# Kernel optimization log

Measured on AMD Instinct MI355X. Metric: run time of the kernel, lower is better.

The kernel has to match this reference:

```python
import jax, jax.numpy as jnp
import numpy as np

B, L, S, D, H = 2, 2048, 2048, 1024, 16
DK = D // H  # d_keys = d_values = 64


def setup_inputs() -> dict:
    key = jax.random.key(0)
    ks = jax.random.split(key, 12)
    sc = 0.02
    return {
        "queries": jax.random.normal(ks[0], (B, L, D), jnp.float32),
        "keys": jax.random.normal(ks[1], (B, S, D), jnp.float32),
        "values": jax.random.normal(ks[2], (B, S, D), jnp.float32),
        "attn_mask": jnp.ones((L, S), dtype=bool),
        "Wq": jax.random.normal(ks[3], (D, H * DK), jnp.float32) * sc,
        "bq": jnp.zeros((H * DK,), jnp.float32),
        "Wk": jax.random.normal(ks[4], (D, H * DK), jnp.float32) * sc,
        "bk": jnp.zeros((H * DK,), jnp.float32),
        "Wv": jax.random.normal(ks[5], (D, H * DK), jnp.float32) * sc,
        "bv": jnp.zeros((H * DK,), jnp.float32),
        "Wo": jax.random.normal(ks[6], (H * DK, D), jnp.float32) * sc,
        "bo": jnp.zeros((D,), jnp.float32),
    }


def reference(queries, keys, values, attn_mask, Wq, bq, Wk, bk, Wv, bv, Wo, bo):
    b, l, _ = queries.shape
    s = keys.shape[1]
    # QKV projections -> [B, T, H, DK]
    q = (queries @ Wq + bq).reshape(b, l, H, DK)
    k = (keys @ Wk + bk).reshape(b, s, H, DK)
    v = (values @ Wv + bv).reshape(b, s, H, DK)
    scale = 1.0 / jnp.sqrt(jnp.asarray(DK, q.dtype))
    # attention scores [B, H, L, S]
    scores = jnp.einsum("blhd,bshd->bhls", q, k) * scale
    scores = jnp.where(attn_mask[None, None, :, :], scores, jnp.finfo(scores.dtype).min)
    attn = jax.nn.softmax(scores, axis=-1)
    out = jnp.einsum("bhls,bshd->blhd", attn, v).reshape(b, l, H * DK)
    out = out @ Wo + bo
    return (out, attn)
```

## Files before the change

### kernel.cpp

```cpp
#include <hip/hip_runtime.h>
#include <hip/hip_bf16.h>


#define BB 2
#define LL 2048
#define SS 2048
#define DD 1024
#define HH 16
#define DKK 64

typedef __bf16 bf16_t;
typedef bf16_t bf16x8 __attribute__((ext_vector_type(8)));
typedef bf16_t bf16x4 __attribute__((ext_vector_type(4)));
typedef float f32x4 __attribute__((ext_vector_type(4)));

static __device__ __forceinline__ f32x4 mfma16(bf16x8 a, bf16x8 b, f32x4 c) {
  return __builtin_amdgcn_mfma_f32_16x16x32_bf16(a, b, c, 0, 0, 0);
}

__global__ void wconv_kernel(const float* __restrict__ Wq, const float* __restrict__ Wk,
                             const float* __restrict__ Wv, const float* __restrict__ Wo,
                             bf16_t* __restrict__ wT) {
  const int which = blockIdx.z;
  const float* W = (which == 0) ? Wq : (which == 1) ? Wk : (which == 2) ? Wv : Wo;
  bf16_t* dst = wT + (size_t)which * 1024 * 1024;
  __shared__ float tile[32][33];
  const int n0 = blockIdx.x * 32, k0 = blockIdx.y * 32;
  const int tx = threadIdx.x, ty = threadIdx.y;
#pragma unroll
  for (int i = 0; i < 4; i++) {
    int k = ty * 4 + i;
    tile[k][tx] = W[(size_t)(k0 + k) * 1024 + n0 + tx];
  }
  __syncthreads();
#pragma unroll
  for (int i = 0; i < 4; i++) {
    int n = ty * 4 + i;
    dst[(size_t)(n0 + n) * 1024 + k0 + tx] = (bf16_t)tile[tx][n];
  }
}

__global__ void aconv_kernel(const float* __restrict__ q, const float* __restrict__ k,
                             const float* __restrict__ v, bf16_t* __restrict__ out) {
  const int which = blockIdx.y;
  const float* src = (which == 0) ? q : (which == 1) ? k : v;
  bf16_t* dst = out + (size_t)which * 4 * 1024 * 1024;
  const size_t i = ((size_t)blockIdx.x * 256 + threadIdx.x) * 4;
  float4 f = *(const float4*)(src + i);
  bf16x4 t;
  t[0] = (bf16_t)f.x; t[1] = (bf16_t)f.y; t[2] = (bf16_t)f.z; t[3] = (bf16_t)f.w;
  *(bf16x4*)(dst + i) = t;
}

__launch_bounds__(256)
__global__ void qkv_gemm_kernel(const bf16_t* __restrict__ abf, const bf16_t* __restrict__ wT,
                                const float* __restrict__ bq, const float* __restrict__ bk,
                                const float* __restrict__ bv, bf16_t* __restrict__ q_ws,
                                bf16_t* __restrict__ k_ws, bf16_t* __restrict__ v_ws) {
  const int which = blockIdx.z;
  const bf16_t* A = abf + (size_t)which * 4 * 1024 * 1024;
  const bf16_t* BT = wT + (size_t)which * 1024 * 1024;
  const float* bias = (which == 0) ? bq : (which == 1) ? bk : bv;
  bf16_t* out = (which == 0) ? q_ws : (which == 1) ? k_ws : v_ws;

  const int n_blk = blockIdx.x * 128, m_blk = blockIdx.y * 128;
  const int lane = threadIdx.x & 63, w = threadIdx.x >> 6;
  const int wm = m_blk + (w >> 1) * 64, wn = n_blk + (w & 1) * 64;
  const int r = lane & 15, quad = lane >> 4;

  f32x4 acc[4][4] = {};
  for (int k0 = 0; k0 < 1024; k0 += 32) {
    const int kq = k0 + quad * 8;
    bf16x8 af[4], bfv[4];
#pragma unroll
    for (int mi = 0; mi < 4; mi++)
      af[mi] = *(const bf16x8*)(A + (size_t)(wm + mi * 16 + r) * 1024 + kq);
#pragma unroll
    for (int ni = 0; ni < 4; ni++)
      bfv[ni] = *(const bf16x8*)(BT + (size_t)(wn + ni * 16 + r) * 1024 + kq);
#pragma unroll
    for (int mi = 0; mi < 4; mi++)
#pragma unroll
      for (int ni = 0; ni < 4; ni++) acc[mi][ni] = mfma16(af[mi], bfv[ni], acc[mi][ni]);
  }
#pragma unroll
  for (int ni = 0; ni < 4; ni++) {
    const int n = wn + ni * 16 + r;
    const float bs = bias[n];
    const int h = n >> 6, d = n & 63;
#pragma unroll
    for (int mi = 0; mi < 4; mi++) {
#pragma unroll
      for (int reg = 0; reg < 4; reg++) {
        const int m = wm + mi * 16 + quad * 4 + reg;
        const int b = m >> 11, t = m & 2047;
        out[((size_t)(b * HH + h) * SS + t) * DKK + d] = (bf16_t)(acc[mi][ni][reg] + bs);
      }
    }
  }
}

__global__ void vtrans_kernel(const bf16_t* __restrict__ v, bf16_t* __restrict__ vT) {
  const int bh = blockIdx.y, s0 = blockIdx.x * 64;
  __shared__ bf16_t tile[64][68];
  const int t = threadIdx.x;
  {
    const int row = t >> 2, cb = (t & 3) * 16;
    const bf16_t* src = v + ((size_t)bh * SS + s0 + row) * DKK + cb;
#pragma unroll
    for (int i = 0; i < 16; i++) tile[row][cb + i] = src[i];
  }
  __syncthreads();
  {
    const int d = t >> 2, sb = (t & 3) * 16;
    bf16_t* dst = vT + ((size_t)bh * DKK + d) * SS + s0 + sb;
#pragma unroll
    for (int i = 0; i < 16; i++) dst[i] = tile[sb + i][d];
  }
}

__launch_bounds__(256, 4)
__global__ void attn_kernel(const bf16_t* __restrict__ q_ws, const bf16_t* __restrict__ k_ws,
                            const bf16_t* __restrict__ vT_ws, float* __restrict__ attn_out,
                            bf16_t* __restrict__ ao_ws) {
  const int lin = blockIdx.x;
  const int xcd = lin & 7;
  const int idx = lin >> 3;
  const int bh = (xcd << 2) | (idx >> 5);
  const int xblk = idx & 31;
  const int b = bh >> 4, h = bh & 15;
  const int tid = threadIdx.x, lane = tid & 63, w = tid >> 6;
  const int r = lane & 15, quad = lane >> 4;
  const int q0 = (xblk * 4 + w) * 16;

  __shared__ bf16_t p_lds_all[4][16][272];
  bf16_t(*p_lds)[272] = p_lds_all[w];

  const float Kl = 0.125f * 1.44269504f;

  bf16x8 aq[2];
  {
    const bf16_t* qrow = q_ws + ((size_t)bh * LL + q0 + r) * DKK + quad * 8;
    aq[0] = *(const bf16x8*)(qrow);
    aq[1] = *(const bf16x8*)(qrow + 32);
  }
  const bf16_t* kbase = k_ws + (size_t)bh * SS * DKK;
  const bf16_t* vtb = vT_ws + (size_t)bh * DKK * SS;

  float m[4] = {-3e38f, -3e38f, -3e38f, -3e38f};
  float sa[4] = {0.f, 0.f, 0.f, 0.f};
  for (int ch = 0; ch < 8; ch++) {
    const int sbase = ch * 256;
    f32x4 sc[16];
#pragma unroll
    for (int c = 0; c < 16; c++) sc[c] = (f32x4){0.f, 0.f, 0.f, 0.f};
#pragma unroll
    for (int c = 0; c < 16; c++) {
      const bf16_t* kp = kbase + (size_t)(sbase + c * 16 + r) * DKK + quad * 8;
      sc[c] = mfma16(aq[0], *(const bf16x8*)kp, sc[c]);
      sc[c] = mfma16(aq[1], *(const bf16x8*)(kp + 32), sc[c]);
    }
#pragma unroll
    for (int reg = 0; reg < 4; reg++) {
      float cm = sc[0][reg];
#pragma unroll
      for (int c = 1; c < 16; c++) cm = fmaxf(cm, sc[c][reg]);
      const float mn = fmaxf(m[reg], cm);
      const float mKl = mn * Kl;
      float acc = 0.f;
#pragma unroll
      for (int c = 0; c < 16; c++) acc += __builtin_amdgcn_exp2f(sc[c][reg] * Kl - mKl);
      sa[reg] = sa[reg] * __builtin_amdgcn_exp2f((m[reg] - mn) * Kl) + acc;
      m[reg] = mn;
    }
  }
#pragma unroll
  for (int off = 1; off < 16; off <<= 1) {
#pragma unroll
    for (int reg = 0; reg < 4; reg++) {
      const float mo = __shfl_xor(m[reg], off, 64);
      const float so = __shfl_xor(sa[reg], off, 64);
      const float mn = fmaxf(m[reg], mo);
      sa[reg] = sa[reg] * __builtin_amdgcn_exp2f((m[reg] - mn) * Kl) +
                so * __builtin_amdgcn_exp2f((mo - mn) * Kl);
      m[reg] = mn;
    }
  }
  float C2[4];
#pragma unroll
  for (int reg = 0; reg < 4; reg++) C2[reg] = m[reg] * Kl + __builtin_amdgcn_logf(sa[reg]);

  f32x4 oacc[4];
#pragma unroll
  for (int ni = 0; ni < 4; ni++) oacc[ni] = (f32x4){0.f, 0.f, 0.f, 0.f};
  float* aout = attn_out + ((size_t)bh * LL + q0) * SS;

  for (int ch = 0; ch < 8; ch++) {
    const int sbase = ch * 256;
    f32x4 sc[16];
#pragma unroll
    for (int c = 0; c < 16; c++) sc[c] = (f32x4){0.f, 0.f, 0.f, 0.f};
#pragma unroll
    for (int c = 0; c < 16; c++) {
      const bf16_t* kp = kbase + (size_t)(sbase + c * 16 + r) * DKK + quad * 8;
      sc[c] = mfma16(aq[0], *(const bf16x8*)kp, sc[c]);
      sc[c] = mfma16(aq[1], *(const bf16x8*)(kp + 32), sc[c]);
    }
#pragma unroll
    for (int c = 0; c < 16; c++) {
#pragma unroll
      for (int reg = 0; reg < 4; reg++) {
        const float p = __builtin_amdgcn_exp2f(sc[c][reg] * Kl - C2[reg]);
        p_lds[quad * 4 + reg][c * 16 + r] = (bf16_t)p;
      }
    }
#pragma unroll
    for (int row = 0; row < 16; row++) {
      bf16x4 t = *(const bf16x4*)(&p_lds[row][lane * 4]);
      f32x4 f;
      f[0] = (float)t[0]; f[1] = (float)t[1]; f[2] = (float)t[2]; f[3] = (float)t[3];
      __builtin_nontemporal_store(f, (f32x4*)(aout + (size_t)row * SS + sbase + lane * 4));
    }
#pragma unroll
    for (int ks = 0; ks < 8; ks++) {
      bf16x8 ap = *(const bf16x8*)(&p_lds[r][ks * 32 + quad * 8]);
#pragma unroll
      for (int ni = 0; ni < 4; ni++) {
        bf16x8 bv = *(const bf16x8*)(vtb + (size_t)(ni * 16 + r) * SS + sbase + ks * 32 + quad * 8);
        oacc[ni] = mfma16(ap, bv, oacc[ni]);
      }
    }
  }
#pragma unroll
  for (int ni = 0; ni < 4; ni++) {
#pragma unroll
    for (int reg = 0; reg < 4; reg++) {
      const int row = quad * 4 + reg;
      ao_ws[((size_t)b * LL + q0 + row) * DD + h * DKK + ni * 16 + r] = (bf16_t)oacc[ni][reg];
    }
  }
}

__launch_bounds__(256)
__global__ void out_gemm_kernel(const bf16_t* __restrict__ A, const bf16_t* __restrict__ BT,
                                const float* __restrict__ bias, float* __restrict__ out) {
  const int n_blk = blockIdx.x * 128, m_blk = blockIdx.y * 64;
  const int lane = threadIdx.x & 63, w = threadIdx.x >> 6;
  const int wm = m_blk + (w >> 1) * 32, wn = n_blk + (w & 1) * 64;
  const int r = lane & 15, quad = lane >> 4;
  f32x4 acc[2][4] = {};
  for (int k0 = 0; k0 < 1024; k0 += 32) {
    const int kq = k0 + quad * 8;
    bf16x8 af[2], bfv[4];
#pragma unroll
    for (int mi = 0; mi < 2; mi++)
      af[mi] = *(const bf16x8*)(A + (size_t)(wm + mi * 16 + r) * 1024 + kq);
#pragma unroll
    for (int ni = 0; ni < 4; ni++)
      bfv[ni] = *(const bf16x8*)(BT + (size_t)(wn + ni * 16 + r) * 1024 + kq);
#pragma unroll
    for (int mi = 0; mi < 2; mi++)
#pragma unroll
      for (int ni = 0; ni < 4; ni++) acc[mi][ni] = mfma16(af[mi], bfv[ni], acc[mi][ni]);
  }
#pragma unroll
  for (int ni = 0; ni < 4; ni++) {
    const int n = wn + ni * 16 + r;
    const float bs = bias[n];
#pragma unroll
    for (int mi = 0; mi < 2; mi++) {
#pragma unroll
      for (int reg = 0; reg < 4; reg++) {
        const int m = wm + mi * 16 + quad * 4 + reg;
        out[(size_t)m * 1024 + n] = acc[mi][ni][reg] + bs;
      }
    }
  }
}

extern "C" void kernel_launch(void* const* d_in, const int* in_sizes, int n_in,
                              void* d_out, int out_size, void* d_ws, size_t ws_size,
                              hipStream_t stream) {
  const float* queries = (const float*)d_in[0];
  const float* keys = (const float*)d_in[1];
  const float* values = (const float*)d_in[2];
  const float* Wq = (const float*)d_in[4];
  const float* bq = (const float*)d_in[5];
  const float* Wk = (const float*)d_in[6];
  const float* bk = (const float*)d_in[7];
  const float* Wv = (const float*)d_in[8];
  const float* bv = (const float*)d_in[9];
  const float* Wo = (const float*)d_in[10];
  const float* bo = (const float*)d_in[11];

  float* out = (float*)d_out;
  float* attn_out = out + (size_t)BB * LL * DD;

  const size_t M = 1u << 20;
  bf16_t* wT = (bf16_t*)d_ws;
  bf16_t* q_ws = wT + 4 * M;
  bf16_t* k_ws = q_ws + 4 * M;
  bf16_t* v_ws = k_ws + 4 * M;
  bf16_t* X = v_ws + 4 * M;
  bf16_t* abf = X;
  bf16_t* vT_ws = X;
  bf16_t* ao_ws = X + 4 * M;

  hipLaunchKernelGGL(wconv_kernel, dim3(32, 32, 4), dim3(32, 8), 0, stream, Wq, Wk, Wv, Wo, wT);
  hipLaunchKernelGGL(aconv_kernel, dim3(4096, 3), dim3(256), 0, stream, queries, keys, values, abf);
  hipLaunchKernelGGL(qkv_gemm_kernel, dim3(8, 32, 3), dim3(256), 0, stream, abf, wT, bq, bk, bv,
                     q_ws, k_ws, v_ws);
  hipLaunchKernelGGL(vtrans_kernel, dim3(32, 32), dim3(256), 0, stream, v_ws, vT_ws);
  hipLaunchKernelGGL(attn_kernel, dim3(1024), dim3(256), 0, stream, q_ws, k_ws, vT_ws,
                     attn_out, ao_ws);
  hipLaunchKernelGGL(out_gemm_kernel, dim3(8, 64), dim3(256), 0, stream, ao_ws, wT + 3 * M, bo, out);
}
```

Before: 1.036 ms.

## Stage K and V tiles in LDS with async double-buffered loads

The attention kernel now shares K and V^T tiles across the block's four waves. Tiles of 64 keys are loaded into double-buffered LDS with global_load_lds, instead of each wave reading K and V^T from global memory on its own. The K projection and V transpose write their outputs in an XOR-swizzled layout so the LDS reads avoid bank conflicts. It also replaces the nontemporal attention-probability stores with normal stores, shrinks the per-wave P buffer, and lowers launch bounds occupancy from 4 to 3. The cost is a block-wide barrier every chunk and more LDS use per block.

```diff
diff --git a/kernel.cpp b/kernel.cpp
--- a/kernel.cpp
+++ b/kernel.cpp
@@ -16,6 +16,11 @@
 
 static __device__ __forceinline__ f32x4 mfma16(bf16x8 a, bf16x8 b, f32x4 c) {
   return __builtin_amdgcn_mfma_f32_16x16x32_bf16(a, b, c, 0, 0, 0);
+}
+
+static __device__ __forceinline__ void gl16(const bf16_t* g, bf16_t* l) {
+  __builtin_amdgcn_global_load_lds((const __attribute__((address_space(1))) void*)g,
+                                   (__attribute__((address_space(3))) void*)l, 16, 0, 0);
 }
 
 __global__ void wconv_kernel(const float* __restrict__ Wq, const float* __restrict__ Wk,
@@ -62,6 +67,7 @@
   const bf16_t* BT = wT + (size_t)which * 1024 * 1024;
   const float* bias = (which == 0) ? bq : (which == 1) ? bk : bv;
   bf16_t* out = (which == 0) ? q_ws : (which == 1) ? k_ws : v_ws;
+  const bool kswz = (which == 1);
 
   const int n_blk = blockIdx.x * 128, m_blk = blockIdx.y * 128;
   const int lane = threadIdx.x & 63, w = threadIdx.x >> 6;
@@ -94,7 +100,8 @@
       for (int reg = 0; reg < 4; reg++) {
         const int m = wm + mi * 16 + quad * 4 + reg;
         const int b = m >> 11, t = m & 2047;
-        out[((size_t)(b * HH + h) * SS + t) * DKK + d] = (bf16_t)(acc[mi][ni][reg] + bs);
+        const int dw = kswz ? ((((d >> 3) ^ (t & 7)) << 3) | (d & 7)) : d;
+        out[((size_t)(b * HH + h) * SS + t) * DKK + dw] = (bf16_t)(acc[mi][ni][reg] + bs);
       }
     }
   }
@@ -112,14 +119,21 @@
   }
   __syncthreads();
   {
-    const int d = t >> 2, sb = (t & 3) * 16;
-    bf16_t* dst = vT + ((size_t)bh * DKK + d) * SS + s0 + sb;
-#pragma unroll
-    for (int i = 0; i < 16; i++) dst[i] = tile[sb + i][d];
-  }
-}
-
-__launch_bounds__(256, 4)
+    const int d = t >> 2;
+    bf16_t* dstrow = vT + ((size_t)bh * DKK + d) * SS + s0;
+#pragma unroll
+    for (int ib = 0; ib < 2; ib++) {
+      const int bblk = (t & 3) * 2 + ib;
+      const int bs = bblk ^ (d & 7);
+      bf16x8 tmp;
+#pragma unroll
+      for (int j = 0; j < 8; j++) tmp[j] = tile[bblk * 8 + j][d];
+      *(bf16x8*)(dstrow + bs * 8) = tmp;
+    }
+  }
+}
+
+__launch_bounds__(256, 3)
 __global__ void attn_kernel(const bf16_t* __restrict__ q_ws, const bf16_t* __restrict__ k_ws,
                             const bf16_t* __restrict__ vT_ws, float* __restrict__ attn_out,
                             bf16_t* __restrict__ ao_ws) {
@@ -133,8 +147,10 @@
   const int r = lane & 15, quad = lane >> 4;
   const int q0 = (xblk * 4 + w) * 16;
 
-  __shared__ bf16_t p_lds_all[4][16][272];
-  bf16_t(*p_lds)[272] = p_lds_all[w];
+  __shared__ bf16_t kbuf[2][64 * 64];
+  __shared__ bf16_t vbuf[2][64 * 64];
+  __shared__ bf16_t p_all[4][16][72];
+  bf16_t(*p_lds)[72] = p_all[w];
 
   const float Kl = 0.125f * 1.44269504f;
 
@@ -147,32 +163,50 @@
   const bf16_t* kbase = k_ws + (size_t)bh * SS * DKK;
   const bf16_t* vtb = vT_ws + (size_t)bh * DKK * SS;
 
+  const int kb0 = (quad ^ (r & 7)) << 3;
+  const int kb1 = ((quad + 4) ^ (r & 7)) << 3;
+
   float m[4] = {-3e38f, -3e38f, -3e38f, -3e38f};
   float sa[4] = {0.f, 0.f, 0.f, 0.f};
-  for (int ch = 0; ch < 8; ch++) {
-    const int sbase = ch * 256;
-    f32x4 sc[16];
-#pragma unroll
-    for (int c = 0; c < 16; c++) sc[c] = (f32x4){0.f, 0.f, 0.f, 0.f};
-#pragma unroll
-    for (int c = 0; c < 16; c++) {
-      const bf16_t* kp = kbase + (size_t)(sbase + c * 16 + r) * DKK + quad * 8;
-      sc[c] = mfma16(aq[0], *(const bf16x8*)kp, sc[c]);
-      sc[c] = mfma16(aq[1], *(const bf16x8*)(kp + 32), sc[c]);
+
+  {
+    const bf16_t* ksrc = kbase + (size_t)tid * 8;
+    gl16(ksrc, &kbuf[0][tid * 8]);
+    gl16(ksrc + 2048, &kbuf[0][tid * 8 + 2048]);
+  }
+  __syncthreads();
+  for (int ch = 0; ch < 32; ch++) {
+    const int cur = ch & 1;
+    if (ch + 1 < 32) {
+      const bf16_t* ksrc = kbase + (size_t)(ch + 1) * 4096 + tid * 8;
+      gl16(ksrc, &kbuf[cur ^ 1][tid * 8]);
+      gl16(ksrc + 2048, &kbuf[cur ^ 1][tid * 8 + 2048]);
+    }
+    f32x4 sc[4];
+#pragma unroll
+    for (int c = 0; c < 4; c++) sc[c] = (f32x4){0.f, 0.f, 0.f, 0.f};
+#pragma unroll
+    for (int c = 0; c < 4; c++) {
+      const int rr = c * 16 + r;
+      bf16x8 k0 = *(const bf16x8*)&kbuf[cur][rr * 64 + kb0];
+      bf16x8 k1 = *(const bf16x8*)&kbuf[cur][rr * 64 + kb1];
+      sc[c] = mfma16(aq[0], k0, sc[c]);
+      sc[c] = mfma16(aq[1], k1, sc[c]);
     }
 #pragma unroll
     for (int reg = 0; reg < 4; reg++) {
       float cm = sc[0][reg];
 #pragma unroll
-      for (int c = 1; c < 16; c++) cm = fmaxf(cm, sc[c][reg]);
+      for (int c = 1; c < 4; c++) cm = fmaxf(cm, sc[c][reg]);
       const float mn = fmaxf(m[reg], cm);
       const float mKl = mn * Kl;
       float acc = 0.f;
 #pragma unroll
-      for (int c = 0; c < 16; c++) acc += __builtin_amdgcn_exp2f(sc[c][reg] * Kl - mKl);
+      for (int c = 0; c < 4; c++) acc += __builtin_amdgcn_exp2f(sc[c][reg] * Kl - mKl);
       sa[reg] = sa[reg] * __builtin_amdgcn_exp2f((m[reg] - mn) * Kl) + acc;
       m[reg] = mn;
     }
+    __syncthreads();
   }
 #pragma unroll
   for (int off = 1; off < 16; off <<= 1) {
@@ -193,43 +227,66 @@
   f32x4 oacc[4];
 #pragma unroll
   for (int ni = 0; ni < 4; ni++) oacc[ni] = (f32x4){0.f, 0.f, 0.f, 0.f};
-  float* aout = attn_out + ((size_t)bh * LL + q0) * SS;
-
-  for (int ch = 0; ch < 8; ch++) {
-    const int sbase = ch * 256;
-    f32x4 sc[16];
-#pragma unroll
-    for (int c = 0; c < 16; c++) sc[c] = (f32x4){0.f, 0.f, 0.f, 0.f};
-#pragma unroll
-    for (int c = 0; c < 16; c++) {
-      const bf16_t* kp = kbase + (size_t)(sbase + c * 16 + r) * DKK + quad * 8;
-      sc[c] = mfma16(aq[0], *(const bf16x8*)kp, sc[c]);
-      sc[c] = mfma16(aq[1], *(const bf16x8*)(kp + 32), sc[c]);
-    }
-#pragma unroll
-    for (int c = 0; c < 16; c++) {
+  float* aoutb = attn_out + ((size_t)bh * LL + q0) * SS;
+
+  {
+    const bf16_t* ksrc = kbase + (size_t)tid * 8;
+    gl16(ksrc, &kbuf[0][tid * 8]);
+    gl16(ksrc + 2048, &kbuf[0][tid * 8 + 2048]);
+    const bf16_t* vsrc = vtb + (size_t)(tid >> 3) * SS + (tid & 7) * 8;
+    gl16(vsrc, &vbuf[0][tid * 8]);
+    gl16(vsrc + 32 * SS, &vbuf[0][tid * 8 + 2048]);
+  }
+  __syncthreads();
+  for (int ch = 0; ch < 32; ch++) {
+    const int cur = ch & 1;
+    if (ch + 1 < 32) {
+      const bf16_t* ksrc = kbase + (size_t)(ch + 1) * 4096 + tid * 8;
+      gl16(ksrc, &kbuf[cur ^ 1][tid * 8]);
+      gl16(ksrc + 2048, &kbuf[cur ^ 1][tid * 8 + 2048]);
+      const bf16_t* vsrc = vtb + (size_t)(tid >> 3) * SS + (ch + 1) * 64 + (tid & 7) * 8;
+      gl16(vsrc, &vbuf[cur ^ 1][tid * 8]);
+      gl16(vsrc + 32 * SS, &vbuf[cur ^ 1][tid * 8 + 2048]);
+    }
+    f32x4 sc[4];
+#pragma unroll
+    for (int c = 0; c < 4; c++) sc[c] = (f32x4){0.f, 0.f, 0.f, 0.f};
+#pragma unroll
+    for (int c = 0; c < 4; c++) {
+      const int rr = c * 16 + r;
+      bf16x8 k0 = *(const bf16x8*)&kbuf[cur][rr * 64 + kb0];
+      bf16x8 k1 = *(const bf16x8*)&kbuf[cur][rr * 64 + kb1];
+      sc[c] = mfma16(aq[0], k0, sc[c]);
+      sc[c] = mfma16(aq[1], k1, sc[c]);
+    }
+#pragma unroll
+    for (int c = 0; c < 4; c++) {
 #pragma unroll
       for (int reg = 0; reg < 4; reg++) {
         const float p = __builtin_amdgcn_exp2f(sc[c][reg] * Kl - C2[reg]);
         p_lds[quad * 4 + reg][c * 16 + r] = (bf16_t)p;
       }
     }
-#pragma unroll
-    for (int row = 0; row < 16; row++) {
-      bf16x4 t = *(const bf16x4*)(&p_lds[row][lane * 4]);
+    float* aout = aoutb + ch * 64;
+#pragma unroll
+    for (int rg = 0; rg < 4; rg++) {
+      const int row = rg * 4 + quad;
+      bf16x4 t4 = *(const bf16x4*)&p_lds[row][r * 4];
       f32x4 f;
-      f[0] = (float)t[0]; f[1] = (float)t[1]; f[2] = (float)t[2]; f[3] = (float)t[3];
-      __builtin_nontemporal_store(f, (f32x4*)(aout + (size_t)row * SS + sbase + lane * 4));
-    }
-#pragma unroll
-    for (int ks = 0; ks < 8; ks++) {
-      bf16x8 ap = *(const bf16x8*)(&p_lds[r][ks * 32 + quad * 8]);
+      f[0] = (float)t4[0]; f[1] = (float)t4[1]; f[2] = (float)t4[2]; f[3] = (float)t4[3];
+      *(f32x4*)(aout + (size_t)row * SS + r * 4) = f;
+    }
+#pragma unroll
+    for (int ks = 0; ks < 2; ks++) {
+      bf16x8 ap = *(const bf16x8*)&p_lds[r][ks * 32 + quad * 8];
 #pragma unroll
       for (int ni = 0; ni < 4; ni++) {
-        bf16x8 bv = *(const bf16x8*)(vtb + (size_t)(ni * 16 + r) * SS + sbase + ks * 32 + quad * 8);
+        const int d = ni * 16 + r;
+        bf16x8 bv = *(const bf16x8*)&vbuf[cur][d * 64 + ((((ks * 4 + quad) ^ (r & 7))) << 3)];
         oacc[ni] = mfma16(ap, bv, oacc[ni]);
       }
     }
+    __syncthreads();
   }
 #pragma unroll
   for (int ni = 0; ni < 4; ni++) {
```

After: 862.0 us. -16.8%, faster.
